# Kernel optimization log

Hardware: AMD Instinct MI355X
Metric: run time of the kernel (lower is better)

The kernel has to match this reference:

```python
import jax, jax.numpy as jnp
import numpy as np

B, LQ, LK, D = 16, 2048, 2048, 256
NEG = -1e10


def setup_inputs() -> dict:
    key = jax.random.key(0)
    k1, k2, k3, k4, k5 = jax.random.split(key, 5)
    scale = 1.0 / np.sqrt(D)
    return {
        "x": jax.random.normal(k1, (B, LQ, D), dtype=jnp.float32),
        "y": jax.random.normal(k2, (B, LK, D), dtype=jnp.float32),
        "mask": jnp.zeros((B, LK), dtype=bool),  # True = padded key position
        "Wq": jax.random.normal(k3, (D, D), dtype=jnp.float32) * scale,
        "Wk": jax.random.normal(k4, (D, D), dtype=jnp.float32) * scale,
        "Wv": jax.random.normal(k5, (D, D), dtype=jnp.float32) * scale,
    }


def reference(x, y, mask, Wq, Wk, Wv):
    # nn.Linear: out = in @ W.T (no bias)
    q = jnp.einsum('bqd,ed->bqe', x, Wq)   # [B, LQ, D]
    k = jnp.einsum('bkd,ed->bke', y, Wk)   # [B, LK, D]
    v = jnp.einsum('bkd,ed->bke', y, Wv)   # [B, LK, D]
    # cdist (p=2) via GEMM expansion: ||q||^2 + ||k||^2 - 2 q.k
    qn = jnp.sum(q * q, axis=-1)                              # [B, LQ]
    kn = jnp.sum(k * k, axis=-1)                              # [B, LK]
    d2 = qn[:, :, None] + kn[:, None, :] - 2.0 * jnp.einsum('bqd,bkd->bqk', q, k)
    dist = jnp.sqrt(jnp.maximum(d2, 0.0))                     # [B, LQ, LK]
    scores = jnp.exp(-dist)
    # masked_fill: where original mask is True, set pre-softmax score to -1e10
    scores = jnp.where(mask[:, None, :], NEG, scores)
    attn = jax.nn.softmax(scores, axis=-1)                    # [B, LQ, LK]
    att_out = jnp.einsum('bqk,bkd->bqd', attn, v)             # [B, LQ, D]
    return (att_out, attn)
```

## Files before the change

### kernel.cpp

```cpp
#include <hip/hip_runtime.h>
#include <stdint.h>

#define B_   16
#define L_   2048
#define D_   256
#define NROW (B_*L_)

#define EPAD 40
#define TPAD 66

typedef __attribute__((ext_vector_type(8))) short s8v;
typedef __attribute__((ext_vector_type(4))) float f4v;
typedef __attribute__((ext_vector_type(4))) float f4n;

__device__ __forceinline__ unsigned short f2b(float f) {
    unsigned u = __builtin_bit_cast(unsigned, f);
    return (unsigned short)((u + 0x7fffu + ((u >> 16) & 1u)) >> 16);
}

__device__ __forceinline__ unsigned cvtpk(float a, float b) {
    unsigned r;
    asm("v_cvt_pk_bf16_f32 %0, %1, %2" : "=v"(r) : "v"(a), "v"(b));
    return r;
}

__device__ __forceinline__ void gl16(const void* g, void* l) {
    __builtin_amdgcn_global_load_lds(
        (const __attribute__((address_space(1))) unsigned int*)g,
        (__attribute__((address_space(3))) unsigned int*)l, 16, 0, 0);
}

template<int N> __device__ __forceinline__ void waitbar() {
    asm volatile("s_waitcnt vmcnt(%0)\n\ts_barrier" :: "i"(N) : "memory");
}
__device__ __forceinline__ void barOnly() {
    asm volatile("s_barrier" ::: "memory");
}

__global__ __launch_bounds__(256) void wconv_kernel(
    const float* __restrict__ Wq, const float* __restrict__ Wk,
    const float* __restrict__ Wv, unsigned short* __restrict__ Wb)
{
    const int t  = threadIdx.x;
    const int r0 = blockIdx.x * 64;
    const int wt = blockIdx.y;
    const float* W = wt == 0 ? Wq : (wt == 1 ? Wk : Wv);
    unsigned short* O = Wb + (size_t)wt * 256 * 256;
    #pragma unroll
    for (int p = 0; p < 16; ++p) {
        int idx  = p*256 + t;
        int row  = r0 + (idx >> 6);
        int half = idx & 1;
        int blk  = (idx & 63) >> 1;
        int c4   = blk*8 + half*4;
        float4 v = *(const float4*)(W + (size_t)row*D_ + c4);
        uint2 pw; pw.x = cvtpk(v.x, v.y); pw.y = cvtpk(v.z, v.w);
        *(uint2*)(O + row*256 + (blk ^ (row & 15))*8 + half*4) = pw;
    }
}

__device__ __forceinline__ void stage_W(const unsigned short* Wsrc, unsigned short* buf,
                                        int e0h, int w, int lane) {
    #pragma unroll
    for (int p = 0; p < 4; ++p) {
        int slot = p*256 + w*64 + lane;
        int row  = slot >> 5;
        int blk  = slot & 31;
        gl16(Wsrc + (size_t)(e0h + row)*256 + blk*8,
             buf + (size_t)(p*256 + w*64)*8);
    }
}

__global__ __launch_bounds__(256) void qkv_kernel(
    const float* __restrict__ x, const float* __restrict__ y,
    const unsigned short* __restrict__ Wb,
    unsigned short* __restrict__ Qb, unsigned short* __restrict__ Kb,
    unsigned short* __restrict__ Vt,
    float* __restrict__ qn, float* __restrict__ kn)
{
    __shared__ unsigned short Xs[64*256];
    __shared__ unsigned short Wsb[2][32*256];
    __shared__ unsigned short Ts[64*TPAD];

    const int t    = threadIdx.x;
    const int r0   = blockIdx.x * 64;
    const int type = blockIdx.y;
    const float* X = type ? y : x;

    #pragma unroll
    for (int p = 0; p < 16; ++p) {
        int idx  = p*256 + t;
        int row  = idx >> 6;
        int half = idx & 1;
        int blk  = (idx & 63) >> 1;
        int c4   = blk*8 + half*4;
        float4 vx = *(const float4*)(X + (size_t)(r0+row)*D_ + c4);
        uint2 px; px.x = cvtpk(vx.x, vx.y); px.y = cvtpk(vx.z, vx.w);
        *(uint2*)(Xs + row*256 + (blk ^ (row & 15))*8 + half*4) = px;
    }

    const int w = t >> 6, lane = t & 63, q16 = lane & 15, quad = lane >> 4;
    const int m0 = w * 16;

    const unsigned short* W0 = Wb + (type ? 65536 : 0);
    const unsigned short* W1 = Wb + 131072;

    stage_W(W0, Wsb[0], 0,  w, lane);
    stage_W(W0, Wsb[1], 32, w, lane);

    asm volatile("s_waitcnt vmcnt(4) lgkmcnt(0)\n\ts_barrier" ::: "memory");

    s8v xa[8];
    #pragma unroll
    for (int c = 0; c < 8; ++c)
        xa[c] = *(const s8v*)(Xs + (m0 + q16)*256 + (((c*4+quad) ^ q16)*8));

    float p4[4] = {0.f, 0.f, 0.f, 0.f};
    const f4v z4 = {0.f, 0.f, 0.f, 0.f};
    f4v acc[4];

    auto compute_half = [&](int par) {
        #pragma unroll
        for (int c = 0; c < 8; ++c)
            #pragma unroll
            for (int nn = 0; nn < 2; ++nn) {
                s8v bb = *(const s8v*)(Wsb[par] + (nn*16 + q16)*256 + (((c*4+quad) ^ q16)*8));
                acc[par*2+nn] = __builtin_amdgcn_mfma_f32_16x16x32_bf16(xa[c], bb, acc[par*2+nn], 0, 0, 0);
            }
    };

    auto epi_qk = [&](int ct) {
        unsigned short* Out = type ? Kb : Qb;
        #pragma unroll
        for (int n = 0; n < 4; ++n)
            #pragma unroll
            for (int r = 0; r < 4; ++r) {
                float v = acc[n][r];
                p4[r] += v * v;
                Out[(size_t)(r0 + m0 + quad*4 + r)*D_ + ct*64 + n*16 + q16] = f2b(v);
            }
    };

    auto epi_v = [&](int ct) {
        #pragma unroll
        for (int n = 0; n < 4; ++n)
            #pragma unroll
            for (int r = 0; r < 4; ++r)
                Ts[(m0 + quad*4 + r)*TPAD + n*16 + q16] = f2b(acc[n][r]);
        asm volatile("s_waitcnt lgkmcnt(0)\n\ts_barrier" ::: "memory");
        int j = t >> 2, kseg = t & 3;
        unsigned pk[8];
        #pragma unroll
        for (int i = 0; i < 8; ++i) {
            unsigned lo = Ts[(kseg*16 + 2*i    )*TPAD + j];
            unsigned hi = Ts[(kseg*16 + 2*i + 1)*TPAD + j];
            pk[i] = lo | (hi << 16);
        }
        int bb_ = r0 >> 11, k0g = r0 & (L_ - 1);
        unsigned short* dst = Vt + (size_t)(bb_*D_ + ct*64 + j)*L_ + k0g + kseg*16;
        *(uint4*)dst       = make_uint4(pk[0], pk[1], pk[2], pk[3]);
        *((uint4*)dst + 1) = make_uint4(pk[4], pk[5], pk[6], pk[7]);
    };

    if (!type) {
        #pragma unroll
        for (int h = 0; h < 8; ++h) {
            if (h == 7)      waitbar<0>();
            else if (h > 0) { if (h & 1) waitbar<4>(); else waitbar<20>(); }
            const int par = h & 1;
            acc[par*2] = z4; acc[par*2+1] = z4;
            compute_half(par);
            if (par) epi_qk(h >> 1);
            barOnly();
            if (h + 2 < 8) stage_W(W0, Wsb[par], (h+2)*32, w, lane);
        }
    } else {
        #pragma unroll
        for (int h = 0; h < 16; ++h) {
            if (h == 15)     waitbar<0>();
            else if (h > 0) {
                if (h & 1)       waitbar<4>();
                else if (h <= 8) waitbar<20>();
                else             waitbar<6>();
            }
            const int par = h & 1;
            acc[par*2] = z4; acc[par*2+1] = z4;
            compute_half(par);
            if (par) { if (h < 8) epi_qk(h >> 1); else epi_v((h - 8) >> 1); }
            barOnly();
            if (h + 2 < 16) {
                const unsigned short* Ws_ = (h + 2 < 8) ? W0 : W1;
                stage_W(Ws_, Wsb[par], ((h + 2) & 7) * 32, w, lane);
            }
        }
    }

    {
        float* norm = type ? kn : qn;
        #pragma unroll
        for (int r = 0; r < 4; ++r) {
            float v = p4[r];
            v += __shfl_xor(v, 1, 16);
            v += __shfl_xor(v, 2, 16);
            v += __shfl_xor(v, 4, 16);
            v += __shfl_xor(v, 8, 16);
            if (q16 == 0) norm[r0 + m0 + quad*4 + r] = v;
        }
    }
}

__device__ __forceinline__ void stage_K(const unsigned short* Kb, unsigned short* ks,
                                        int bk, int k0, int w, int lane) {
    #pragma unroll
    for (int p = 0; p < 2; ++p) {
        int slot = p*512 + w*64 + lane;
        int row  = slot >> 5;
        int blk  = slot & 31;
        gl16(Kb + (size_t)(bk + k0 + row)*D_ + ((blk ^ (row & 15))*8),
             ks + (size_t)(p*512 + w*64)*8);
    }
}
__device__ __forceinline__ void stage_V(const unsigned short* Vt, unsigned short* vs,
                                        int bD, int k0, int w, int lane) {
    #pragma unroll
    for (int p = 0; p < 2; ++p) {
        int slot = p*512 + w*64 + lane;
        int d    = slot >> 2;
        int blk  = slot & 3;
        gl16(Vt + (size_t)(bD + d)*L_ + k0 + ((blk ^ ((d >> 1) & 3))*8),
             vs + (size_t)(p*512 + w*64)*8);
    }
}

__global__ __launch_bounds__(512) void attnpv_kernel(
    const unsigned short* __restrict__ Qb, const unsigned short* __restrict__ Kb,
    const unsigned short* __restrict__ Vt,
    const float* __restrict__ qn, const float* __restrict__ kn,
    const unsigned char* __restrict__ mask,
    unsigned short* __restrict__ Eb,
    float* __restrict__ rowsum, float* __restrict__ att_out)
{
    __shared__ unsigned short Ks[3][32*256];
    __shared__ unsigned short Vs[3][256*32];
    __shared__ unsigned short Es[8][16*EPAD];
    __shared__ float         knS[L_];
    __shared__ unsigned char mkS[L_];

    const int t  = threadIdx.x;
    const int s  = blockIdx.y * 16 + blockIdx.x;
    const int b  = ((s & 7) << 1) | (s >> 7);
    const int q0 = ((s >> 3) & 15) * 128;
    const int bk = b * L_;
    const int bD = b * D_;
    const int w = t >> 6, lane = t & 63, q16 = lane & 15, quad = lane >> 4;
    const int qrow = bk + q0 + w*16;

    *(float4*)&knS[t*4] = *(const float4*)&kn[bk + t*4];
    ((unsigned*)mkS)[t] = ((const unsigned*)(mask + bk))[t];

    s8v qa[8];
    float qnr[4];
    #pragma unroll
    for (int c = 0; c < 8; ++c)
        qa[c] = *(const s8v*)(Qb + (size_t)(qrow + q16)*D_ + c*32 + quad*8);
    #pragma unroll
    for (int r = 0; r < 4; ++r)
        qnr[r] = qn[qrow + quad*4 + r];

    unsigned short* ebase = Eb + (size_t)(qrow + (lane >> 2))*L_ + (lane & 3)*8;
    const unsigned short* esrc = &Es[w][(lane >> 2)*EPAD + (lane & 3)*8];

    float rs[4] = {0.f, 0.f, 0.f, 0.f};
    const f4v z4 = {0.f, 0.f, 0.f, 0.f};
    f4v O[16];
    #pragma unroll
    for (int n = 0; n < 16; ++n) O[n] = z4;

    auto do_tile = [&](int kt, int cur) {
        const int k0 = kt * 32;
        float kcv[2]; int mkv[2];
        #pragma unroll
        for (int n = 0; n < 2; ++n) {
            kcv[n] = knS[k0 + n*16 + q16];
            mkv[n] = mkS[k0 + n*16 + q16];
        }
        #pragma unroll
        for (int n = 0; n < 2; ++n) {
            f4v s4 = z4;
            __builtin_amdgcn_s_setprio(1);
            #pragma unroll
            for (int c = 0; c < 8; ++c) {
                s8v bb = *(const s8v*)(Ks[cur] + (n*16 + q16)*256 + (((c*4+quad) ^ q16)*8));
                s4 = __builtin_amdgcn_mfma_f32_16x16x32_bf16(qa[c], bb, s4, 0, 0, 0);
            }
            __builtin_amdgcn_s_setprio(0);
            #pragma unroll
            for (int r = 0; r < 4; ++r) {
                float d2 = fmaf(-2.0f, s4[r], qnr[r] + kcv[n]);
                float dist = sqrtf(fmaxf(d2, 0.f));
                float E = mkv[n] ? 0.f : __expf(__expf(-dist));
                rs[r] += E;
                Es[w][(quad*4 + r)*EPAD + n*16 + q16] = f2b(E);
            }
        }
        *(s8v*)(ebase + k0) = *(const s8v*)esrc;
        s8v af = *(const s8v*)(&Es[w][q16*EPAD + quad*8]);
        __builtin_amdgcn_s_setprio(1);
        #pragma unroll
        for (int n = 0; n < 16; ++n) {
            s8v vb = *(const s8v*)(Vs[cur] + (n*16 + q16)*32 +
                                   ((quad ^ ((q16 >> 1) & 3))*8));
            O[n] = __builtin_amdgcn_mfma_f32_16x16x32_bf16(af, vb, O[n], 0, 0, 0);
        }
        __builtin_amdgcn_s_setprio(0);
    };

    stage_K(Kb, Ks[0], bk, 0,  w, lane);  stage_V(Vt, Vs[0], bD, 0,  w, lane);
    stage_K(Kb, Ks[1], bk, 32, w, lane);  stage_V(Vt, Vs[1], bD, 32, w, lane);

    asm volatile("s_waitcnt vmcnt(4) lgkmcnt(0)\n\ts_barrier" ::: "memory");
    do_tile(0, 0);
    asm volatile("s_barrier" ::: "memory");
    stage_K(Kb, Ks[2], bk, 64, w, lane);  stage_V(Vt, Vs[2], bD, 64, w, lane);

    int cur = 1;
    for (int kt = 1; kt <= 62; ++kt) {
        asm volatile("s_waitcnt vmcnt(5)\n\ts_barrier" ::: "memory");
        do_tile(kt, cur);
        asm volatile("s_barrier" ::: "memory");
        if (kt <= 61) {
            int nb = cur - 1; if (nb < 0) nb = 2;
            stage_K(Kb, Ks[nb], bk, (kt+2)*32, w, lane);
            stage_V(Vt, Vs[nb], bD, (kt+2)*32, w, lane);
        }
        cur = (cur == 2) ? 0 : cur + 1;
    }
    asm volatile("s_waitcnt vmcnt(1)\n\ts_barrier" ::: "memory");
    do_tile(63, 0);

    float inv4[4];
    #pragma unroll
    for (int r = 0; r < 4; ++r) {
        float v = rs[r];
        v += __shfl_xor(v, 1, 16);
        v += __shfl_xor(v, 2, 16);
        v += __shfl_xor(v, 4, 16);
        v += __shfl_xor(v, 8, 16);
        inv4[r] = 1.0f / v;
        if (q16 == 0) rowsum[qrow + quad*4 + r] = v;
    }
    #pragma unroll
    for (int n = 0; n < 16; ++n)
        #pragma unroll
        for (int r = 0; r < 4; ++r)
            __builtin_nontemporal_store(O[n][r] * inv4[r],
                att_out + (size_t)(qrow + quad*4 + r)*D_ + n*16 + q16);
}

__global__ __launch_bounds__(256) void norm_kernel(
    const unsigned short* __restrict__ Eb,
    const float* __restrict__ rowsum,
    float* __restrict__ attn_out)
{
    const int row = blockIdx.x;
    const int t   = threadIdx.x;
    const float inv = 1.0f / rowsum[row];
    const size_t base = (size_t)row * L_ + t*8;

    s8v e = *(const s8v*)(Eb + base);
    f4n o0, o1;
    o0.x = __builtin_bit_cast(float, ((unsigned)(unsigned short)e[0]) << 16) * inv;
    o0.y = __builtin_bit_cast(float, ((unsigned)(unsigned short)e[1]) << 16) * inv;
    o0.z = __builtin_bit_cast(float, ((unsigned)(unsigned short)e[2]) << 16) * inv;
    o0.w = __builtin_bit_cast(float, ((unsigned)(unsigned short)e[3]) << 16) * inv;
    o1.x = __builtin_bit_cast(float, ((unsigned)(unsigned short)e[4]) << 16) * inv;
    o1.y = __builtin_bit_cast(float, ((unsigned)(unsigned short)e[5]) << 16) * inv;
    o1.z = __builtin_bit_cast(float, ((unsigned)(unsigned short)e[6]) << 16) * inv;
    o1.w = __builtin_bit_cast(float, ((unsigned)(unsigned short)e[7]) << 16) * inv;
    __builtin_nontemporal_store(o0, (f4n*)(attn_out + base));
    __builtin_nontemporal_store(o1, (f4n*)(attn_out + base + 4));
}

extern "C" void kernel_launch(void* const* d_in, const int* in_sizes, int n_in,
                              void* d_out, int out_size, void* d_ws, size_t ws_size,
                              hipStream_t stream) {
    (void)in_sizes; (void)n_in; (void)out_size; (void)ws_size;
    const float* x  = (const float*)d_in[0];
    const float* y  = (const float*)d_in[1];
    const unsigned char* mask = (const unsigned char*)d_in[2];
    const float* Wq = (const float*)d_in[3];
    const float* Wk = (const float*)d_in[4];
    const float* Wv = (const float*)d_in[5];

    char* ws = (char*)d_ws;
    unsigned short* Qb = (unsigned short*)ws;
    unsigned short* Kb = Qb + (size_t)NROW * D_;
    unsigned short* Vt = Kb + (size_t)NROW * D_;
    float* qn     = (float*)(ws + 3 * (size_t)NROW * D_ * 2);
    float* kn     = qn + NROW;
    float* rowsum = kn + NROW;
    unsigned short* Eb = (unsigned short*)(rowsum + NROW);
    unsigned short* Wb = Eb + (size_t)NROW * L_;

    float* att_out = (float*)d_out;
    float* attn    = att_out + (size_t)NROW * D_;

    wconv_kernel<<<dim3(4, 3), 256, 0, stream>>>(Wq, Wk, Wv, Wb);
    qkv_kernel<<<dim3(512, 2), 256, 0, stream>>>(x, y, Wb, Qb, Kb, Vt, qn, kn);
    attnpv_kernel<<<dim3(16, 16), 512, 0, stream>>>(Qb, Kb, Vt, qn, kn, mask,
                                                    Eb, rowsum, att_out);
    norm_kernel<<<dim3(NROW), 256, 0, stream>>>(Eb, rowsum, attn);
}
```

Measured before the change: 566.2 us.

## Drop per-tile second barrier, prefetch before compute, split QK MFMA chains

The K/V prefetch for tile kt+2 now goes out right after the top-of-loop barrier, before the tile's compute, instead of after a second barrier. This cuts one workgroup barrier per key tile and gives the loads more time to overlap with compute, and the triple buffer keeps the slot being overwritten separate from the one in use. The QK^T MFMA loop now runs four independent accumulator chains, which are summed afterwards, to shorten dependent MFMA latency. The bf16 E tile stores and the norm kernel's loads become nontemporal. The vmcnt wait counts were re-tuned, so the prefetch schedule depends on every outstanding-memory count being right.

New measurement: 564.3 us. Within noise of the previous version (-0.3%).

```diff
diff --git a/kernel.cpp b/kernel.cpp
--- a/kernel.cpp
+++ b/kernel.cpp
@@ -276,39 +276,47 @@
     #pragma unroll
     for (int n = 0; n < 16; ++n) O[n] = z4;
 
-    auto do_tile = [&](int kt, int cur) {
-        const int k0 = kt * 32;
+    auto do_tile = [&](int k0, const unsigned short* ksb, const unsigned short* vsb) {
         float kcv[2]; int mkv[2];
         #pragma unroll
         for (int n = 0; n < 2; ++n) {
             kcv[n] = knS[k0 + n*16 + q16];
             mkv[n] = mkS[k0 + n*16 + q16];
         }
-        #pragma unroll
-        for (int n = 0; n < 2; ++n) {
-            f4v s4 = z4;
-            __builtin_amdgcn_s_setprio(1);
-            #pragma unroll
-            for (int c = 0; c < 8; ++c) {
-                s8v bb = *(const s8v*)(Ks[cur] + (n*16 + q16)*256 + (((c*4+quad) ^ q16)*8));
-                s4 = __builtin_amdgcn_mfma_f32_16x16x32_bf16(qa[c], bb, s4, 0, 0, 0);
-            }
-            __builtin_amdgcn_s_setprio(0);
+        f4v sA0 = z4, sA1 = z4, sB0 = z4, sB1 = z4;
+        __builtin_amdgcn_s_setprio(1);
+        #pragma unroll
+        for (int c = 0; c < 4; ++c) {
+            const int c0 = 2*c, c1 = 2*c + 1;
+            s8v bA0 = *(const s8v*)(ksb + (q16      )*256 + (((c0*4+quad) ^ q16)*8));
+            s8v bA1 = *(const s8v*)(ksb + (16 + q16 )*256 + (((c0*4+quad) ^ q16)*8));
+            s8v bB0 = *(const s8v*)(ksb + (q16      )*256 + (((c1*4+quad) ^ q16)*8));
+            s8v bB1 = *(const s8v*)(ksb + (16 + q16 )*256 + (((c1*4+quad) ^ q16)*8));
+            sA0 = __builtin_amdgcn_mfma_f32_16x16x32_bf16(qa[c0], bA0, sA0, 0, 0, 0);
+            sA1 = __builtin_amdgcn_mfma_f32_16x16x32_bf16(qa[c0], bA1, sA1, 0, 0, 0);
+            sB0 = __builtin_amdgcn_mfma_f32_16x16x32_bf16(qa[c1], bB0, sB0, 0, 0, 0);
+            sB1 = __builtin_amdgcn_mfma_f32_16x16x32_bf16(qa[c1], bB1, sB1, 0, 0, 0);
+        }
+        __builtin_amdgcn_s_setprio(0);
+        f4v s4n[2];
+        s4n[0] = sA0 + sB0;
+        s4n[1] = sA1 + sB1;
+        #pragma unroll
+        for (int n = 0; n < 2; ++n)
             #pragma unroll
             for (int r = 0; r < 4; ++r) {
-                float d2 = fmaf(-2.0f, s4[r], qnr[r] + kcv[n]);
+                float d2 = fmaf(-2.0f, s4n[n][r], qnr[r] + kcv[n]);
                 float dist = sqrtf(fmaxf(d2, 0.f));
                 float E = mkv[n] ? 0.f : __expf(__expf(-dist));
                 rs[r] += E;
                 Es[w][(quad*4 + r)*EPAD + n*16 + q16] = f2b(E);
             }
-        }
-        *(s8v*)(ebase + k0) = *(const s8v*)esrc;
+        __builtin_nontemporal_store(*(const s8v*)esrc, (s8v*)(ebase + k0));
         s8v af = *(const s8v*)(&Es[w][q16*EPAD + quad*8]);
         __builtin_amdgcn_s_setprio(1);
         #pragma unroll
         for (int n = 0; n < 16; ++n) {
-            s8v vb = *(const s8v*)(Vs[cur] + (n*16 + q16)*32 +
+            s8v vb = *(const s8v*)(vsb + (n*16 + q16)*32 +
                                    ((quad ^ ((q16 >> 1) & 3))*8));
             O[n] = __builtin_amdgcn_mfma_f32_16x16x32_bf16(af, vb, O[n], 0, 0, 0);
         }
@@ -317,26 +325,23 @@
 
     stage_K(Kb, Ks[0], bk, 0,  w, lane);  stage_V(Vt, Vs[0], bD, 0,  w, lane);
     stage_K(Kb, Ks[1], bk, 32, w, lane);  stage_V(Vt, Vs[1], bD, 32, w, lane);
-
     asm volatile("s_waitcnt vmcnt(4) lgkmcnt(0)\n\ts_barrier" ::: "memory");
-    do_tile(0, 0);
-    asm volatile("s_barrier" ::: "memory");
     stage_K(Kb, Ks[2], bk, 64, w, lane);  stage_V(Vt, Vs[2], bD, 64, w, lane);
+    do_tile(0, Ks[0], Vs[0]);
 
     int cur = 1;
-    for (int kt = 1; kt <= 62; ++kt) {
+    for (int kt = 1; kt < 63; ++kt) {
         asm volatile("s_waitcnt vmcnt(5)\n\ts_barrier" ::: "memory");
-        do_tile(kt, cur);
-        asm volatile("s_barrier" ::: "memory");
-        if (kt <= 61) {
-            int nb = cur - 1; if (nb < 0) nb = 2;
+        if (kt < 62) {
+            int nb = cur + 2; if (nb >= 3) nb -= 3;
             stage_K(Kb, Ks[nb], bk, (kt+2)*32, w, lane);
             stage_V(Vt, Vs[nb], bD, (kt+2)*32, w, lane);
         }
+        do_tile(kt*32, Ks[cur], Vs[cur]);
         cur = (cur == 2) ? 0 : cur + 1;
     }
-    asm volatile("s_waitcnt vmcnt(1)\n\ts_barrier" ::: "memory");
-    do_tile(63, 0);
+    asm volatile("s_waitcnt vmcnt(2)\n\ts_barrier" ::: "memory");
+    do_tile(63*32, Ks[0], Vs[0]);
 
     float inv4[4];
     #pragma unroll
@@ -367,7 +372,7 @@
     const float inv = 1.0f / rowsum[row];
     const size_t base = (size_t)row * L_ + t*8;
 
-    s8v e = *(const s8v*)(Eb + base);
+    s8v e = __builtin_nontemporal_load((const s8v*)(Eb + base));
     f4n o0, o1;
     o0.x = __builtin_bit_cast(float, ((unsigned)(unsigned short)e[0]) << 16) * inv;
     o0.y = __builtin_bit_cast(float, ((unsigned)(unsigned short)e[1]) << 16) * inv;
```

## Split key range across blocks and process two query bands per wave

Applied to the files above, without the earlier changes.

The attention kernel now splits the key dimension into two halves, each handled by a separate block, and each wave handles 32 query rows (two 16-row bands) so every K/V fragment read from LDS feeds two MFMAs. Partial row sums and unnormalized outputs for each half go to workspace, and the norm kernel combines them and normalizes both att_out and attn. This aims to raise MFMA reuse of shared-memory K/V and shorten each block's serial loop. The cost is extra global traffic for the fp32 partial outputs, higher register pressure from the doubled accumulators (launch bounds now request 2 blocks), and a larger workspace. E stores and loads also become nontemporal.

Result: slower. 594.5 us (+5.0%).

```diff
diff --git a/kernel.cpp b/kernel.cpp
--- a/kernel.cpp
+++ b/kernel.cpp
@@ -210,164 +210,180 @@
 }
 
 __device__ __forceinline__ void stage_K(const unsigned short* Kb, unsigned short* ks,
-                                        int bk, int k0, int w, int lane) {
+                                        int kb0, int k0, int w, int lane) {
     #pragma unroll
     for (int p = 0; p < 2; ++p) {
         int slot = p*512 + w*64 + lane;
         int row  = slot >> 5;
         int blk  = slot & 31;
-        gl16(Kb + (size_t)(bk + k0 + row)*D_ + ((blk ^ (row & 15))*8),
+        gl16(Kb + (size_t)(kb0 + k0 + row)*D_ + ((blk ^ (row & 15))*8),
              ks + (size_t)(p*512 + w*64)*8);
     }
 }
 __device__ __forceinline__ void stage_V(const unsigned short* Vt, unsigned short* vs,
-                                        int bD, int k0, int w, int lane) {
+                                        int bD, int kg0, int w, int lane) {
     #pragma unroll
     for (int p = 0; p < 2; ++p) {
         int slot = p*512 + w*64 + lane;
         int d    = slot >> 2;
         int blk  = slot & 3;
-        gl16(Vt + (size_t)(bD + d)*L_ + k0 + ((blk ^ ((d >> 1) & 3))*8),
+        gl16(Vt + (size_t)(bD + d)*L_ + kg0 + ((blk ^ ((d >> 1) & 3))*8),
              vs + (size_t)(p*512 + w*64)*8);
     }
 }
 
-__global__ __launch_bounds__(512) void attnpv_kernel(
+__global__ __launch_bounds__(512, 2) void attnpv_kernel(
     const unsigned short* __restrict__ Qb, const unsigned short* __restrict__ Kb,
     const unsigned short* __restrict__ Vt,
     const float* __restrict__ qn, const float* __restrict__ kn,
     const unsigned char* __restrict__ mask,
     unsigned short* __restrict__ Eb,
-    float* __restrict__ rowsum, float* __restrict__ att_out)
+    float* __restrict__ rs2, float* __restrict__ Op)
 {
     __shared__ unsigned short Ks[3][32*256];
     __shared__ unsigned short Vs[3][256*32];
-    __shared__ unsigned short Es[8][16*EPAD];
-    __shared__ float         knS[L_];
-    __shared__ unsigned char mkS[L_];
+    __shared__ unsigned short Es[8][32*EPAD];
+    __shared__ float         knS[1024];
+    __shared__ unsigned int  mkS4[256];
 
     const int t  = threadIdx.x;
     const int s  = blockIdx.y * 16 + blockIdx.x;
     const int b  = ((s & 7) << 1) | (s >> 7);
-    const int q0 = ((s >> 3) & 15) * 128;
+    const int kh = (s >> 3) & 1;
+    const int q0 = ((s >> 4) & 7) * 256;
     const int bk = b * L_;
+    const int kb0 = bk + kh * 1024;
     const int bD = b * D_;
     const int w = t >> 6, lane = t & 63, q16 = lane & 15, quad = lane >> 4;
-    const int qrow = bk + q0 + w*16;
-
-    *(float4*)&knS[t*4] = *(const float4*)&kn[bk + t*4];
-    ((unsigned*)mkS)[t] = ((const unsigned*)(mask + bk))[t];
-
-    s8v qa[8];
-    float qnr[4];
-    #pragma unroll
-    for (int c = 0; c < 8; ++c)
-        qa[c] = *(const s8v*)(Qb + (size_t)(qrow + q16)*D_ + c*32 + quad*8);
-    #pragma unroll
-    for (int r = 0; r < 4; ++r)
-        qnr[r] = qn[qrow + quad*4 + r];
-
-    unsigned short* ebase = Eb + (size_t)(qrow + (lane >> 2))*L_ + (lane & 3)*8;
-    const unsigned short* esrc = &Es[w][(lane >> 2)*EPAD + (lane & 3)*8];
-
-    float rs[4] = {0.f, 0.f, 0.f, 0.f};
+    const int qrow = bk + q0 + w*32;
+
+    *(float2*)&knS[t*2] = *(const float2*)&kn[kb0 + t*2];
+    if (t < 256) mkS4[t] = *(const unsigned int*)(mask + kb0 + t*4);
+
+    s8v qa[2][8];
+    float qnr[2][4];
+    #pragma unroll
+    for (int band = 0; band < 2; ++band) {
+        #pragma unroll
+        for (int c = 0; c < 8; ++c)
+            qa[band][c] = *(const s8v*)(Qb + (size_t)(qrow + band*16 + q16)*D_ + c*32 + quad*8);
+        #pragma unroll
+        for (int r = 0; r < 4; ++r)
+            qnr[band][r] = qn[qrow + band*16 + quad*4 + r];
+    }
+
+    unsigned short* ebase0 = Eb + (size_t)(qrow + (lane >> 2))*L_ + kh*1024 + (lane & 3)*8;
+    unsigned short* ebase1 = ebase0 + (size_t)16*L_;
+    const unsigned short* esrc0 = &Es[w][(lane >> 2)*EPAD + (lane & 3)*8];
+    const unsigned short* esrc1 = esrc0 + 16*EPAD;
+
+    float rs[2][4] = {{0.f,0.f,0.f,0.f},{0.f,0.f,0.f,0.f}};
     const f4v z4 = {0.f, 0.f, 0.f, 0.f};
-    f4v O[16];
-    #pragma unroll
-    for (int n = 0; n < 16; ++n) O[n] = z4;
-
-    auto do_tile = [&](int kt, int cur) {
+    f4v O[2][16];
+    #pragma unroll
+    for (int band = 0; band < 2; ++band)
+        #pragma unroll
+        for (int n = 0; n < 16; ++n) O[band][n] = z4;
+
+    auto do_tile = [&](int kt, const unsigned short* ksb, const unsigned short* vsb) {
         const int k0 = kt * 32;
         float kcv[2]; int mkv[2];
         #pragma unroll
         for (int n = 0; n < 2; ++n) {
             kcv[n] = knS[k0 + n*16 + q16];
-            mkv[n] = mkS[k0 + n*16 + q16];
-        }
-        #pragma unroll
-        for (int n = 0; n < 2; ++n) {
-            f4v s4 = z4;
-            __builtin_amdgcn_s_setprio(1);
-            #pragma unroll
-            for (int c = 0; c < 8; ++c) {
-                s8v bb = *(const s8v*)(Ks[cur] + (n*16 + q16)*256 + (((c*4+quad) ^ q16)*8));
-                s4 = __builtin_amdgcn_mfma_f32_16x16x32_bf16(qa[c], bb, s4, 0, 0, 0);
+            mkv[n] = ((const unsigned char*)mkS4)[k0 + n*16 + q16];
+        }
+        f4v S[2][2];
+        S[0][0] = z4; S[0][1] = z4; S[1][0] = z4; S[1][1] = z4;
+        __builtin_amdgcn_s_setprio(1);
+        #pragma unroll
+        for (int c = 0; c < 8; ++c)
+            #pragma unroll
+            for (int n = 0; n < 2; ++n) {
+                s8v bb = *(const s8v*)(ksb + (n*16 + q16)*256 + (((c*4+quad) ^ q16)*8));
+                S[0][n] = __builtin_amdgcn_mfma_f32_16x16x32_bf16(qa[0][c], bb, S[0][n], 0, 0, 0);
+                S[1][n] = __builtin_amdgcn_mfma_f32_16x16x32_bf16(qa[1][c], bb, S[1][n], 0, 0, 0);
             }
-            __builtin_amdgcn_s_setprio(0);
-            #pragma unroll
-            for (int r = 0; r < 4; ++r) {
-                float d2 = fmaf(-2.0f, s4[r], qnr[r] + kcv[n]);
-                float dist = sqrtf(fmaxf(d2, 0.f));
-                float E = mkv[n] ? 0.f : __expf(__expf(-dist));
-                rs[r] += E;
-                Es[w][(quad*4 + r)*EPAD + n*16 + q16] = f2b(E);
-            }
-        }
-        *(s8v*)(ebase + k0) = *(const s8v*)esrc;
-        s8v af = *(const s8v*)(&Es[w][q16*EPAD + quad*8]);
+        __builtin_amdgcn_s_setprio(0);
+        #pragma unroll
+        for (int band = 0; band < 2; ++band)
+            #pragma unroll
+            for (int n = 0; n < 2; ++n)
+                #pragma unroll
+                for (int r = 0; r < 4; ++r) {
+                    float d2 = fmaf(-2.0f, S[band][n][r], qnr[band][r] + kcv[n]);
+                    float dist = sqrtf(fmaxf(d2, 0.f));
+                    float E = mkv[n] ? 0.f : __expf(__expf(-dist));
+                    rs[band][r] += E;
+                    Es[w][(band*16 + quad*4 + r)*EPAD + n*16 + q16] = f2b(E);
+                }
+        __builtin_nontemporal_store(*(const s8v*)esrc0, (s8v*)(ebase0 + k0));
+        __builtin_nontemporal_store(*(const s8v*)esrc1, (s8v*)(ebase1 + k0));
+        s8v af0 = *(const s8v*)(&Es[w][(q16     )*EPAD + quad*8]);
+        s8v af1 = *(const s8v*)(&Es[w][(16 + q16)*EPAD + quad*8]);
         __builtin_amdgcn_s_setprio(1);
         #pragma unroll
         for (int n = 0; n < 16; ++n) {
-            s8v vb = *(const s8v*)(Vs[cur] + (n*16 + q16)*32 +
+            s8v vb = *(const s8v*)(vsb + (n*16 + q16)*32 +
                                    ((quad ^ ((q16 >> 1) & 3))*8));
-            O[n] = __builtin_amdgcn_mfma_f32_16x16x32_bf16(af, vb, O[n], 0, 0, 0);
+            O[0][n] = __builtin_amdgcn_mfma_f32_16x16x32_bf16(af0, vb, O[0][n], 0, 0, 0);
+            O[1][n] = __builtin_amdgcn_mfma_f32_16x16x32_bf16(af1, vb, O[1][n], 0, 0, 0);
         }
         __builtin_amdgcn_s_setprio(0);
     };
 
-    stage_K(Kb, Ks[0], bk, 0,  w, lane);  stage_V(Vt, Vs[0], bD, 0,  w, lane);
-    stage_K(Kb, Ks[1], bk, 32, w, lane);  stage_V(Vt, Vs[1], bD, 32, w, lane);
-
+    stage_K(Kb, Ks[0], kb0, 0,  w, lane);  stage_V(Vt, Vs[0], bD, kh*1024 + 0,  w, lane);
+    stage_K(Kb, Ks[1], kb0, 32, w, lane);  stage_V(Vt, Vs[1], bD, kh*1024 + 32, w, lane);
     asm volatile("s_waitcnt vmcnt(4) lgkmcnt(0)\n\ts_barrier" ::: "memory");
-    do_tile(0, 0);
-    asm volatile("s_barrier" ::: "memory");
-    stage_K(Kb, Ks[2], bk, 64, w, lane);  stage_V(Vt, Vs[2], bD, 64, w, lane);
-
-    int cur = 1;
-    for (int kt = 1; kt <= 62; ++kt) {
-        asm volatile("s_waitcnt vmcnt(5)\n\ts_barrier" ::: "memory");
-        do_tile(kt, cur);
-        asm volatile("s_barrier" ::: "memory");
-        if (kt <= 61) {
-            int nb = cur - 1; if (nb < 0) nb = 2;
-            stage_K(Kb, Ks[nb], bk, (kt+2)*32, w, lane);
-            stage_V(Vt, Vs[nb], bD, (kt+2)*32, w, lane);
-        }
-        cur = (cur == 2) ? 0 : cur + 1;
-    }
-    asm volatile("s_waitcnt vmcnt(1)\n\ts_barrier" ::: "memory");
-    do_tile(63, 0);
-
-    float inv4[4];
-    #pragma unroll
-    for (int r = 0; r < 4; ++r) {
-        float v = rs[r];
-        v += __shfl_xor(v, 1, 16);
-        v += __shfl_xor(v, 2, 16);
-        v += __shfl_xor(v, 4, 16);
-        v += __shfl_xor(v, 8, 16);
-        inv4[r] = 1.0f / v;
-        if (q16 == 0) rowsum[qrow + quad*4 + r] = v;
-    }
-    #pragma unroll
-    for (int n = 0; n < 16; ++n)
-        #pragma unroll
-        for (int r = 0; r < 4; ++r)
-            __builtin_nontemporal_store(O[n][r] * inv4[r],
-                att_out + (size_t)(qrow + quad*4 + r)*D_ + n*16 + q16);
+    stage_K(Kb, Ks[2], kb0, 64, w, lane);  stage_V(Vt, Vs[2], bD, kh*1024 + 64, w, lane);
+    do_tile(0, Ks[0], Vs[0]);
+
+    for (int kt = 1; kt < 31; ++kt) {
+        if (kt == 1) { asm volatile("s_waitcnt vmcnt(6)\n\ts_barrier" ::: "memory"); }
+        else         { asm volatile("s_waitcnt vmcnt(8)\n\ts_barrier" ::: "memory"); }
+        if (kt < 30) {
+            int nb = kt + 2; nb -= (nb >= 3) ? 3 : 0; nb -= (nb >= 3) ? 3 : 0;
+            nb = (kt + 2) % 3;
+            stage_K(Kb, Ks[nb], kb0, (kt+2)*32, w, lane);
+            stage_V(Vt, Vs[nb], bD, kh*1024 + (kt+2)*32, w, lane);
+        }
+        do_tile(kt, Ks[kt % 3], Vs[kt % 3]);
+    }
+    asm volatile("s_waitcnt vmcnt(4)\n\ts_barrier" ::: "memory");
+    do_tile(31, Ks[31 % 3], Vs[31 % 3]);
+
+    #pragma unroll
+    for (int band = 0; band < 2; ++band) {
+        #pragma unroll
+        for (int r = 0; r < 4; ++r) {
+            float v = rs[band][r];
+            v += __shfl_xor(v, 1, 16);
+            v += __shfl_xor(v, 2, 16);
+            v += __shfl_xor(v, 4, 16);
+            v += __shfl_xor(v, 8, 16);
+            if (q16 == 0) rs2[(size_t)kh*NROW + qrow + band*16 + quad*4 + r] = v;
+        }
+        #pragma unroll
+        for (int n = 0; n < 16; ++n)
+            #pragma unroll
+            for (int r = 0; r < 4; ++r)
+                __builtin_nontemporal_store(O[band][n][r],
+                    Op + (size_t)kh*NROW*D_ +
+                        (size_t)(qrow + band*16 + quad*4 + r)*D_ + n*16 + q16);
+    }
 }
 
 __global__ __launch_bounds__(256) void norm_kernel(
     const unsigned short* __restrict__ Eb,
-    const float* __restrict__ rowsum,
-    float* __restrict__ attn_out)
+    const float* __restrict__ rs2, const float* __restrict__ Op,
+    float* __restrict__ att_out, float* __restrict__ attn_out)
 {
     const int row = blockIdx.x;
     const int t   = threadIdx.x;
-    const float inv = 1.0f / rowsum[row];
+    const float inv = 1.0f / (rs2[row] + rs2[NROW + row]);
     const size_t base = (size_t)row * L_ + t*8;
 
-    s8v e = *(const s8v*)(Eb + base);
+    s8v e = __builtin_nontemporal_load((const s8v*)(Eb + base));
     f4n o0, o1;
     o0.x = __builtin_bit_cast(float, ((unsigned)(unsigned short)e[0]) << 16) * inv;
     o0.y = __builtin_bit_cast(float, ((unsigned)(unsigned short)e[1]) << 16) * inv;
@@ -379,6 +395,18 @@
     o1.w = __builtin_bit_cast(float, ((unsigned)(unsigned short)e[7]) << 16) * inv;
     __builtin_nontemporal_store(o0, (f4n*)(attn_out + base));
     __builtin_nontemporal_store(o1, (f4n*)(attn_out + base + 4));
+
+    if (t < 32) {
+        const size_t ob = (size_t)row * D_ + t*8;
+        f4n a0 = *(const f4n*)(Op + ob);
+        f4n a1 = *(const f4n*)(Op + ob + 4);
+        f4n b0 = *(const f4n*)(Op + (size_t)NROW*D_ + ob);
+        f4n b1 = *(const f4n*)(Op + (size_t)NROW*D_ + ob + 4);
+        f4n r0_ = (a0 + b0) * inv;
+        f4n r1_ = (a1 + b1) * inv;
+        __builtin_nontemporal_store(r0_, (f4n*)(att_out + ob));
+        __builtin_nontemporal_store(r1_, (f4n*)(att_out + ob + 4));
+    }
 }
 
 extern "C" void kernel_launch(void* const* d_in, const int* in_sizes, int n_in,
@@ -396,11 +424,12 @@
     unsigned short* Qb = (unsigned short*)ws;
     unsigned short* Kb = Qb + (size_t)NROW * D_;
     unsigned short* Vt = Kb + (size_t)NROW * D_;
-    float* qn     = (float*)(ws + 3 * (size_t)NROW * D_ * 2);
-    float* kn     = qn + NROW;
-    float* rowsum = kn + NROW;
-    unsigned short* Eb = (unsigned short*)(rowsum + NROW);
-    unsigned short* Wb = Eb + (size_t)NROW * L_;
+    float* qn  = (float*)(ws + 3 * (size_t)NROW * D_ * 2);
+    float* kn  = qn + NROW;
+    float* rs2 = kn + NROW;
+    unsigned short* Eb = (unsigned short*)(rs2 + 2*(size_t)NROW);
+    float* Op = (float*)(Eb + (size_t)NROW * L_);
+    unsigned short* Wb = (unsigned short*)(Op + 2*(size_t)NROW*D_);
 
     float* att_out = (float*)d_out;
     float* attn    = att_out + (size_t)NROW * D_;
@@ -408,6 +437,6 @@
     wconv_kernel<<<dim3(4, 3), 256, 0, stream>>>(Wq, Wk, Wv, Wb);
     qkv_kernel<<<dim3(512, 2), 256, 0, stream>>>(x, y, Wb, Qb, Kb, Vt, qn, kn);
     attnpv_kernel<<<dim3(16, 16), 512, 0, stream>>>(Qb, Kb, Vt, qn, kn, mask,
-                                                    Eb, rowsum, att_out);
-    norm_kernel<<<dim3(NROW), 256, 0, stream>>>(Eb, rowsum, attn);
-}
+                                                    Eb, rs2, Op);
+    norm_kernel<<<dim3(NROW), 256, 0, stream>>>(Eb, rs2, Op, att_out, attn);
+}
```
